# Optimization experiments

Hardware: AMD Instinct MI355X
Metric: run time of the kernel (lower is better)

The kernel has to match this reference:

```python
import jax, jax.numpy as jnp
import numpy as np

N_NODES = 100000
N_EDGES = 1000000
C_IN = 64
C_OUT = 64


def setup_inputs() -> dict:
    key = jax.random.key(0)
    k1, k2, k3 = jax.random.split(key, 3)
    x = jax.random.normal(k1, (N_NODES, C_IN), dtype=jnp.float32)
    edge_index = jax.random.randint(k2, (2, N_EDGES), 0, N_NODES, dtype=jnp.int64)
    # glorot-scaled weight, zero bias (as in GCNConv defaults)
    scale = jnp.sqrt(2.0 / (C_IN + C_OUT)).astype(jnp.float32)
    W = jax.random.normal(k3, (C_IN, C_OUT), dtype=jnp.float32) * scale
    b = jnp.zeros((C_OUT,), dtype=jnp.float32)
    return {"x": x, "edge_index": edge_index, "W": W, "b": b}


def reference(x, edge_index, W, b):
    # GCNConv: out = D^{-1/2} (A + I) D^{-1/2} (x W) + b
    n = x.shape[0]
    # add self loops
    loop = jnp.arange(n, dtype=edge_index.dtype)
    src = jnp.concatenate([edge_index[0], loop])  # [E+N]
    dst = jnp.concatenate([edge_index[1], loop])  # [E+N]
    # degree of A_hat computed over destination (col) nodes, edge_weight = 1
    ones = jnp.ones(src.shape[0], dtype=x.dtype)
    deg = jax.ops.segment_sum(ones, dst, num_segments=n)  # [N]
    deg_inv_sqrt = jnp.where(deg > 0, jax.lax.rsqrt(deg), 0.0)
    norm = deg_inv_sqrt[src] * deg_inv_sqrt[dst]  # [E+N]
    # linear transform, then gather-scale-scatter aggregation
    h = x @ W  # [N, C_OUT]
    msg = norm[:, None] * h[src]  # [E+N, C_OUT]
    out = jax.ops.segment_sum(msg, dst, num_segments=n)  # [N, C_OUT]
    return out + b
```

## Files before the change

kernel.cpp:

```cpp
#include <hip/hip_runtime.h>
#include <hip/hip_bf16.h>

#define C 64

__device__ __forceinline__ float bflo(unsigned u) { return __uint_as_float(u << 16); }
__device__ __forceinline__ float bfhi(unsigned u) { return __uint_as_float(u & 0xffff0000u); }
__device__ __forceinline__ unsigned bfrne(float f) {
    unsigned u = __float_as_uint(f);
    return (u + 0x7fffu + ((u >> 16) & 1u)) >> 16;
}

__device__ __forceinline__ unsigned xcc_id() {
    return __builtin_amdgcn_s_getreg(6164) & 7u;
}

__global__ void zero_kernel(uint4* __restrict__ p, int n4) {
    int i = blockIdx.x * blockDim.x + threadIdx.x;
    if (i < n4) p[i] = make_uint4(0u, 0u, 0u, 0u);
}

__global__ void count_part_kernel(const int* __restrict__ dst, unsigned* __restrict__ part,
                                  int S, unsigned* __restrict__ rank, int E) {
    int e = blockIdx.x * blockDim.x + threadIdx.x;
    if (e < E) {
        unsigned x = xcc_id();
        unsigned d = (unsigned)dst[e];
        unsigned r = __hip_atomic_fetch_add(&part[x * (unsigned)S + d], 1u,
                                            __ATOMIC_RELAXED, __HIP_MEMORY_SCOPE_WORKGROUP);
        rank[e] = (x << 27) | r;
    }
}

__global__ void scan1_kernel(unsigned* __restrict__ part, int S,
                             unsigned* __restrict__ deg, unsigned* __restrict__ offs,
                             unsigned* __restrict__ bsum, float* __restrict__ dis, int n) {
    __shared__ unsigned s[256];
    int t = threadIdx.x;
    int base = blockIdx.x * 1024 + t * 4;
    unsigned v0 = 0, v1 = 0, v2 = 0, v3 = 0;
    if (base + 4 <= n) {
        uint4 run = make_uint4(0u, 0u, 0u, 0u);
        #pragma unroll
        for (int x = 0; x < 8; ++x) {
            uint4* p = (uint4*)&part[(size_t)x * S + base];
            uint4 v = *p;
            *p = run;
            run.x += v.x; run.y += v.y; run.z += v.z; run.w += v.w;
        }
        v0 = run.x; v1 = run.y; v2 = run.z; v3 = run.w;
        *(uint4*)&deg[base] = run;
        dis[base + 0] = rsqrtf((float)(v0 + 1u));
        dis[base + 1] = rsqrtf((float)(v1 + 1u));
        dis[base + 2] = rsqrtf((float)(v2 + 1u));
        dis[base + 3] = rsqrtf((float)(v3 + 1u));
    } else if (base < n) {
        for (int j = 0; j < 4; ++j) {
            int i = base + j;
            if (i >= n) break;
            unsigned run = 0;
            #pragma unroll
            for (int x = 0; x < 8; ++x) {
                unsigned* p = &part[(size_t)x * S + i];
                unsigned v = *p;
                *p = run;
                run += v;
            }
            deg[i] = run;
            dis[i] = rsqrtf((float)(run + 1u));
            if (j == 0) v0 = run; else if (j == 1) v1 = run;
            else if (j == 2) v2 = run; else v3 = run;
        }
    }
    s[t] = v0 + v1 + v2 + v3;
    __syncthreads();
    for (int d = 1; d < 256; d <<= 1) {
        unsigned val = (t >= d) ? s[t - d] : 0u;
        __syncthreads();
        s[t] += val;
        __syncthreads();
    }
    unsigned excl = (t == 0) ? 0u : s[t - 1];
    if (t == 255) bsum[blockIdx.x] = s[255];
    if (base + 0 < n) offs[base + 0] = excl;
    if (base + 1 < n) offs[base + 1] = excl + v0;
    if (base + 2 < n) offs[base + 2] = excl + v0 + v1;
    if (base + 3 < n) offs[base + 3] = excl + v0 + v1 + v2;
}

__global__ void scan2_kernel(unsigned* __restrict__ bsum, int nb) {
    __shared__ unsigned s[256];
    int t = threadIdx.x;
    s[t] = (t < nb) ? bsum[t] : 0u;
    __syncthreads();
    for (int d = 1; d < 256; d <<= 1) {
        unsigned val = (t >= d) ? s[t - d] : 0u;
        __syncthreads();
        s[t] += val;
        __syncthreads();
    }
    if (t < nb) bsum[t] = (t == 0) ? 0u : s[t - 1];
}

__global__ void bucket_kernel(const int* __restrict__ src, const int* __restrict__ dst,
                              const unsigned* __restrict__ offs, const unsigned* __restrict__ bsum,
                              const unsigned* __restrict__ part, int S,
                              const unsigned* __restrict__ rank, unsigned* __restrict__ ssrc, int E) {
    int e = blockIdx.x * blockDim.x + threadIdx.x;
    if (e < E) {
        unsigned d = (unsigned)dst[e];
        unsigned u = rank[e];
        unsigned x = u >> 27;
        unsigned pos = offs[d] + bsum[d >> 10] + part[(size_t)x * S + d] + (u & 0x07FFFFFFu);
        ssrc[pos] = (unsigned)src[e];
    }
}

__global__ void __launch_bounds__(256, 4)
gemm64_kernel(const float* __restrict__ x, const float* __restrict__ W,
              const float* __restrict__ dis, unsigned short* __restrict__ hsb, int n) {
    __shared__ float Xl[64][68];
    __shared__ float Wl[64][64];
    int tid = threadIdx.x;
    int rbase = blockIdx.x * 64;
    for (int i = tid; i < 1024; i += 256) {
        ((float4*)Wl)[i] = ((const float4*)W)[i];
    }
    for (int i = tid; i < 1024; i += 256) {
        int r = i >> 4, kq = i & 15;
        float4 v;
        if (rbase + r < n) v = ((const float4*)(x + (size_t)(rbase + r) * C))[kq];
        else               v = make_float4(0.f, 0.f, 0.f, 0.f);
        *(float4*)&Xl[r][kq * 4] = v;
    }
    __syncthreads();

    int tx = tid & 15;
    int ty = tid >> 4;
    float4 acc[4];
    #pragma unroll
    for (int j = 0; j < 4; ++j) acc[j] = make_float4(0.f, 0.f, 0.f, 0.f);

    #pragma unroll 2
    for (int kb = 0; kb < 16; ++kb) {
        float4 wv0 = *(const float4*)&Wl[kb * 4 + 0][tx * 4];
        float4 wv1 = *(const float4*)&Wl[kb * 4 + 1][tx * 4];
        float4 wv2 = *(const float4*)&Wl[kb * 4 + 2][tx * 4];
        float4 wv3 = *(const float4*)&Wl[kb * 4 + 3][tx * 4];
        #pragma unroll
        for (int j = 0; j < 4; ++j) {
            float4 xv = *(const float4*)&Xl[ty * 4 + j][kb * 4];
            acc[j].x = fmaf(xv.x, wv0.x, acc[j].x);
            acc[j].y = fmaf(xv.x, wv0.y, acc[j].y);
            acc[j].z = fmaf(xv.x, wv0.z, acc[j].z);
            acc[j].w = fmaf(xv.x, wv0.w, acc[j].w);
            acc[j].x = fmaf(xv.y, wv1.x, acc[j].x);
            acc[j].y = fmaf(xv.y, wv1.y, acc[j].y);
            acc[j].z = fmaf(xv.y, wv1.z, acc[j].z);
            acc[j].w = fmaf(xv.y, wv1.w, acc[j].w);
            acc[j].x = fmaf(xv.z, wv2.x, acc[j].x);
            acc[j].y = fmaf(xv.z, wv2.y, acc[j].y);
            acc[j].z = fmaf(xv.z, wv2.z, acc[j].z);
            acc[j].w = fmaf(xv.z, wv2.w, acc[j].w);
            acc[j].x = fmaf(xv.w, wv3.x, acc[j].x);
            acc[j].y = fmaf(xv.w, wv3.y, acc[j].y);
            acc[j].z = fmaf(xv.w, wv3.z, acc[j].z);
            acc[j].w = fmaf(xv.w, wv3.w, acc[j].w);
        }
    }
    #pragma unroll
    for (int j = 0; j < 4; ++j) {
        int row = rbase + ty * 4 + j;
        if (row < n) {
            float d = dis[row];
            unsigned p0 = bfrne(acc[j].x * d) | (bfrne(acc[j].y * d) << 16);
            unsigned p1 = bfrne(acc[j].z * d) | (bfrne(acc[j].w * d) << 16);
            ((uint2*)(hsb + (size_t)row * C))[tx] = make_uint2(p0, p1);
        }
    }
}

__global__ void gather_kernel(const unsigned* __restrict__ offs, const unsigned* __restrict__ bsum,
                              const unsigned* __restrict__ deg, const unsigned* __restrict__ ssrc,
                              const float* __restrict__ dis, const unsigned short* __restrict__ hsb,
                              const float* __restrict__ b, float* __restrict__ out, int n) {
    int node = blockIdx.x * 4 + (threadIdx.x >> 6);
    if (node >= n) return;
    int lane = threadIdx.x & 63;
    int g = lane >> 3;
    int l = lane & 7;
    unsigned off = offs[node] + bsum[node >> 10];
    unsigned dg  = deg[node];
    float a0 = 0.f, a1 = 0.f, a2 = 0.f, a3 = 0.f, a4 = 0.f, a5 = 0.f, a6 = 0.f, a7 = 0.f;
    unsigned k = 0;
    for (; k + 16 <= dg; k += 16) {
        unsigned s0 = ssrc[off + k + g];
        unsigned s1 = ssrc[off + k + 8 + g];
        uint4 v0 = ((const uint4*)(hsb + (size_t)s0 * C))[l];
        uint4 v1 = ((const uint4*)(hsb + (size_t)s1 * C))[l];
        a0 += bflo(v0.x) + bflo(v1.x); a1 += bfhi(v0.x) + bfhi(v1.x);
        a2 += bflo(v0.y) + bflo(v1.y); a3 += bfhi(v0.y) + bfhi(v1.y);
        a4 += bflo(v0.z) + bflo(v1.z); a5 += bfhi(v0.z) + bfhi(v1.z);
        a6 += bflo(v0.w) + bflo(v1.w); a7 += bfhi(v0.w) + bfhi(v1.w);
    }
    if (k + 8 <= dg) {
        unsigned s0 = ssrc[off + k + g];
        uint4 v0 = ((const uint4*)(hsb + (size_t)s0 * C))[l];
        a0 += bflo(v0.x); a1 += bfhi(v0.x);
        a2 += bflo(v0.y); a3 += bfhi(v0.y);
        a4 += bflo(v0.z); a5 += bfhi(v0.z);
        a6 += bflo(v0.w); a7 += bfhi(v0.w);
        k += 8;
    }
    if (k + g < dg) {
        unsigned s0 = ssrc[off + k + g];
        uint4 v0 = ((const uint4*)(hsb + (size_t)s0 * C))[l];
        a0 += bflo(v0.x); a1 += bfhi(v0.x);
        a2 += bflo(v0.y); a3 += bfhi(v0.y);
        a4 += bflo(v0.z); a5 += bfhi(v0.z);
        a6 += bflo(v0.w); a7 += bfhi(v0.w);
    }
    #pragma unroll
    for (int m = 8; m <= 32; m <<= 1) {
        a0 += __shfl_xor(a0, m); a1 += __shfl_xor(a1, m);
        a2 += __shfl_xor(a2, m); a3 += __shfl_xor(a3, m);
        a4 += __shfl_xor(a4, m); a5 += __shfl_xor(a5, m);
        a6 += __shfl_xor(a6, m); a7 += __shfl_xor(a7, m);
    }
    if (g < 2) {
        float di = dis[node];
        uint4 u = ((const uint4*)(hsb + (size_t)node * C))[l];
        unsigned w0 = (g == 0) ? u.x : u.z;
        unsigned w1 = (g == 0) ? u.y : u.w;
        float s0 = bflo(w0), s1 = bfhi(w0), s2 = bflo(w1), s3 = bfhi(w1);
        float e0 = (g == 0) ? a0 : a4;
        float e1 = (g == 0) ? a1 : a5;
        float e2 = (g == 0) ? a2 : a6;
        float e3 = (g == 0) ? a3 : a7;
        float4 bv = ((const float4*)b)[l * 2 + g];
        float4 o;
        o.x = di * (s0 + e0) + bv.x;
        o.y = di * (s1 + e1) + bv.y;
        o.z = di * (s2 + e2) + bv.z;
        o.w = di * (s3 + e3) + bv.w;
        ((float4*)(out + (size_t)node * C))[l * 2 + g] = o;
    }
}

extern "C" void kernel_launch(void* const* d_in, const int* in_sizes, int n_in,
                              void* d_out, int out_size, void* d_ws, size_t ws_size,
                              hipStream_t stream) {
    const float* x   = (const float*)d_in[0];
    const int*   ei  = (const int*)d_in[1];
    const float* W   = (const float*)d_in[2];
    const float* b   = (const float*)d_in[3];
    float*       out = (float*)d_out;

    const int N = in_sizes[0] / C;
    const int E = in_sizes[1] / 2;
    const int* src = ei;
    const int* dst = ei + E;

    const int S = (N + 63) & ~63;

    char* ws = (char*)d_ws;
    size_t o = 0;
    auto carve = [&](size_t bytes) { char* p = ws + o; o = (o + bytes + 255) & ~(size_t)255; return p; };
    unsigned* part      = (unsigned*)carve((size_t)8 * S * 4);
    unsigned* deg       = (unsigned*)carve((size_t)N * 4);
    unsigned* offs      = (unsigned*)carve((size_t)N * 4);
    unsigned* bsum      = (unsigned*)carve(1024 * 4);
    float*    dis       = (float*)carve((size_t)N * 4);
    unsigned* rank      = (unsigned*)carve((size_t)E * 4);
    unsigned* ssrc      = (unsigned*)carve((size_t)E * 4);
    unsigned short* hsb = (unsigned short*)carve((size_t)N * C * 2);

    int n4 = 2 * S;
    zero_kernel<<<(n4 + 255) / 256, 256, 0, stream>>>((uint4*)part, n4);

    count_part_kernel<<<(E + 255) / 256, 256, 0, stream>>>(dst, part, S, rank, E);

    int nb = (N + 1023) / 1024;
    scan1_kernel<<<nb, 256, 0, stream>>>(part, S, deg, offs, bsum, dis, N);
    scan2_kernel<<<1, 256, 0, stream>>>(bsum, nb);

    bucket_kernel<<<(E + 255) / 256, 256, 0, stream>>>(src, dst, offs, bsum, part, S, rank, ssrc, E);

    gemm64_kernel<<<(N + 63) / 64, 256, 0, stream>>>(x, W, dis, hsb, N);

    gather_kernel<<<(N + 3) / 4, 256, 0, stream>>>(offs, bsum, deg, ssrc, dis, hsb, b, out, N);
}
```

Before: 131.2 us.

## Fuse CSR build kernels into one cooperative kernel with grid syncs

Merges the zero, count, two scan and bucket kernels into a single cooperative kernel launched with 1024 blocks, using grid.sync between phases instead of separate launches. This is meant to remove four kernel launch gaps and their tail effects. In exchange it adds grid-wide barrier costs and grid-stride loops over fewer threads, and it relies on all 1024 blocks being co-resident.

```diff
diff --git a/kernel.cpp b/kernel.cpp
--- a/kernel.cpp
+++ b/kernel.cpp
@@ -1,7 +1,11 @@
 #include <hip/hip_runtime.h>
 #include <hip/hip_bf16.h>
+#include <hip/hip_cooperative_groups.h>
+
+namespace cg = cooperative_groups;
 
 #define C 64
+#define COOP_BLOCKS 1024
 
 __device__ __forceinline__ float bflo(unsigned u) { return __uint_as_float(u << 16); }
 __device__ __forceinline__ float bfhi(unsigned u) { return __uint_as_float(u & 0xffff0000u); }
@@ -14,99 +18,105 @@
     return __builtin_amdgcn_s_getreg(6164) & 7u;
 }
 
-__global__ void zero_kernel(uint4* __restrict__ p, int n4) {
-    int i = blockIdx.x * blockDim.x + threadIdx.x;
-    if (i < n4) p[i] = make_uint4(0u, 0u, 0u, 0u);
-}
-
-__global__ void count_part_kernel(const int* __restrict__ dst, unsigned* __restrict__ part,
-                                  int S, unsigned* __restrict__ rank, int E) {
-    int e = blockIdx.x * blockDim.x + threadIdx.x;
-    if (e < E) {
+__global__ void __launch_bounds__(256, 8)
+build_kernel(const int* __restrict__ dst, const int* __restrict__ src,
+             unsigned* __restrict__ part, int S,
+             unsigned* __restrict__ rank,
+             unsigned* __restrict__ deg, unsigned* __restrict__ offs,
+             unsigned* __restrict__ bsum, float* __restrict__ dis,
+             unsigned* __restrict__ ssrc, int N, int E) {
+    cg::grid_group grid = cg::this_grid();
+    __shared__ unsigned s[256];
+    int t    = threadIdx.x;
+    int gtid = blockIdx.x * 256 + t;
+    int gsz  = gridDim.x * 256;
+
+    int n4 = 2 * S;
+    for (int i = gtid; i < n4; i += gsz) {
+        ((uint4*)part)[i] = make_uint4(0u, 0u, 0u, 0u);
+    }
+    grid.sync();
+
+    {
         unsigned x = xcc_id();
-        unsigned d = (unsigned)dst[e];
-        unsigned r = __hip_atomic_fetch_add(&part[x * (unsigned)S + d], 1u,
-                                            __ATOMIC_RELAXED, __HIP_MEMORY_SCOPE_WORKGROUP);
-        rank[e] = (x << 27) | r;
-    }
-}
-
-__global__ void scan1_kernel(unsigned* __restrict__ part, int S,
-                             unsigned* __restrict__ deg, unsigned* __restrict__ offs,
-                             unsigned* __restrict__ bsum, float* __restrict__ dis, int n) {
-    __shared__ unsigned s[256];
-    int t = threadIdx.x;
-    int base = blockIdx.x * 1024 + t * 4;
-    unsigned v0 = 0, v1 = 0, v2 = 0, v3 = 0;
-    if (base + 4 <= n) {
-        uint4 run = make_uint4(0u, 0u, 0u, 0u);
-        #pragma unroll
-        for (int x = 0; x < 8; ++x) {
-            uint4* p = (uint4*)&part[(size_t)x * S + base];
-            uint4 v = *p;
-            *p = run;
-            run.x += v.x; run.y += v.y; run.z += v.z; run.w += v.w;
-        }
-        v0 = run.x; v1 = run.y; v2 = run.z; v3 = run.w;
-        *(uint4*)&deg[base] = run;
-        dis[base + 0] = rsqrtf((float)(v0 + 1u));
-        dis[base + 1] = rsqrtf((float)(v1 + 1u));
-        dis[base + 2] = rsqrtf((float)(v2 + 1u));
-        dis[base + 3] = rsqrtf((float)(v3 + 1u));
-    } else if (base < n) {
-        for (int j = 0; j < 4; ++j) {
-            int i = base + j;
-            if (i >= n) break;
-            unsigned run = 0;
+        for (int e = gtid; e < E; e += gsz) {
+            unsigned d = (unsigned)dst[e];
+            unsigned r = __hip_atomic_fetch_add(&part[x * (unsigned)S + d], 1u,
+                                                __ATOMIC_RELAXED, __HIP_MEMORY_SCOPE_WORKGROUP);
+            rank[e] = (x << 27) | r;
+        }
+    }
+    grid.sync();
+
+    int nchunks = (N + 1023) >> 10;
+    for (int c = blockIdx.x; c < nchunks; c += gridDim.x) {
+        int base = c * 1024 + t * 4;
+        unsigned v0 = 0, v1 = 0, v2 = 0, v3 = 0;
+        if (base + 4 <= N) {
+            uint4 run = make_uint4(0u, 0u, 0u, 0u);
             #pragma unroll
             for (int x = 0; x < 8; ++x) {
-                unsigned* p = &part[(size_t)x * S + i];
-                unsigned v = *p;
+                uint4* p = (uint4*)&part[(size_t)x * S + base];
+                uint4 v = *p;
                 *p = run;
-                run += v;
+                run.x += v.x; run.y += v.y; run.z += v.z; run.w += v.w;
             }
-            deg[i] = run;
-            dis[i] = rsqrtf((float)(run + 1u));
-            if (j == 0) v0 = run; else if (j == 1) v1 = run;
-            else if (j == 2) v2 = run; else v3 = run;
-        }
-    }
-    s[t] = v0 + v1 + v2 + v3;
-    __syncthreads();
-    for (int d = 1; d < 256; d <<= 1) {
-        unsigned val = (t >= d) ? s[t - d] : 0u;
+            v0 = run.x; v1 = run.y; v2 = run.z; v3 = run.w;
+            *(uint4*)&deg[base] = run;
+            dis[base + 0] = rsqrtf((float)(v0 + 1u));
+            dis[base + 1] = rsqrtf((float)(v1 + 1u));
+            dis[base + 2] = rsqrtf((float)(v2 + 1u));
+            dis[base + 3] = rsqrtf((float)(v3 + 1u));
+        } else if (base < N) {
+            for (int j = 0; j < 4; ++j) {
+                int i = base + j;
+                if (i >= N) break;
+                unsigned run = 0;
+                #pragma unroll
+                for (int x = 0; x < 8; ++x) {
+                    unsigned* p = &part[(size_t)x * S + i];
+                    unsigned v = *p;
+                    *p = run;
+                    run += v;
+                }
+                deg[i] = run;
+                dis[i] = rsqrtf((float)(run + 1u));
+                if (j == 0) v0 = run; else if (j == 1) v1 = run;
+                else if (j == 2) v2 = run; else v3 = run;
+            }
+        }
+        s[t] = v0 + v1 + v2 + v3;
         __syncthreads();
-        s[t] += val;
+        for (int d = 1; d < 256; d <<= 1) {
+            unsigned val = (t >= d) ? s[t - d] : 0u;
+            __syncthreads();
+            s[t] += val;
+            __syncthreads();
+        }
+        unsigned excl = (t == 0) ? 0u : s[t - 1];
+        if (t == 255) bsum[c] = s[255];
+        if (base + 0 < N) offs[base + 0] = excl;
+        if (base + 1 < N) offs[base + 1] = excl + v0;
+        if (base + 2 < N) offs[base + 2] = excl + v0 + v1;
+        if (base + 3 < N) offs[base + 3] = excl + v0 + v1 + v2;
         __syncthreads();
     }
-    unsigned excl = (t == 0) ? 0u : s[t - 1];
-    if (t == 255) bsum[blockIdx.x] = s[255];
-    if (base + 0 < n) offs[base + 0] = excl;
-    if (base + 1 < n) offs[base + 1] = excl + v0;
-    if (base + 2 < n) offs[base + 2] = excl + v0 + v1;
-    if (base + 3 < n) offs[base + 3] = excl + v0 + v1 + v2;
-}
-
-__global__ void scan2_kernel(unsigned* __restrict__ bsum, int nb) {
-    __shared__ unsigned s[256];
-    int t = threadIdx.x;
-    s[t] = (t < nb) ? bsum[t] : 0u;
-    __syncthreads();
-    for (int d = 1; d < 256; d <<= 1) {
-        unsigned val = (t >= d) ? s[t - d] : 0u;
+    grid.sync();
+
+    if (blockIdx.x == 0) {
+        s[t] = (t < nchunks) ? bsum[t] : 0u;
         __syncthreads();
-        s[t] += val;
-        __syncthreads();
-    }
-    if (t < nb) bsum[t] = (t == 0) ? 0u : s[t - 1];
-}
-
-__global__ void bucket_kernel(const int* __restrict__ src, const int* __restrict__ dst,
-                              const unsigned* __restrict__ offs, const unsigned* __restrict__ bsum,
-                              const unsigned* __restrict__ part, int S,
-                              const unsigned* __restrict__ rank, unsigned* __restrict__ ssrc, int E) {
-    int e = blockIdx.x * blockDim.x + threadIdx.x;
-    if (e < E) {
+        for (int d = 1; d < 256; d <<= 1) {
+            unsigned val = (t >= d) ? s[t - d] : 0u;
+            __syncthreads();
+            s[t] += val;
+            __syncthreads();
+        }
+        if (t < nchunks) bsum[t] = (t == 0) ? 0u : s[t - 1];
+    }
+    grid.sync();
+
+    for (int e = gtid; e < E; e += gsz) {
         unsigned d = (unsigned)dst[e];
         unsigned u = rank[e];
         unsigned x = u >> 27;
@@ -274,16 +284,24 @@
     unsigned* ssrc      = (unsigned*)carve((size_t)E * 4);
     unsigned short* hsb = (unsigned short*)carve((size_t)N * C * 2);
 
-    int n4 = 2 * S;
-    zero_kernel<<<(n4 + 255) / 256, 256, 0, stream>>>((uint4*)part, n4);
-
-    count_part_kernel<<<(E + 255) / 256, 256, 0, stream>>>(dst, part, S, rank, E);
-
-    int nb = (N + 1023) / 1024;
-    scan1_kernel<<<nb, 256, 0, stream>>>(part, S, deg, offs, bsum, dis, N);
-    scan2_kernel<<<1, 256, 0, stream>>>(bsum, nb);
-
-    bucket_kernel<<<(E + 255) / 256, 256, 0, stream>>>(src, dst, offs, bsum, part, S, rank, ssrc, E);
+    {
+        const int*  dst_a  = dst;
+        const int*  src_a  = src;
+        unsigned*   part_a = part;
+        int         S_a    = S;
+        unsigned*   rank_a = rank;
+        unsigned*   deg_a  = deg;
+        unsigned*   offs_a = offs;
+        unsigned*   bsum_a = bsum;
+        float*      dis_a  = dis;
+        unsigned*   ssrc_a = ssrc;
+        int         N_a    = N;
+        int         E_a    = E;
+        void* args[] = { &dst_a, &src_a, &part_a, &S_a, &rank_a, &deg_a,
+                         &offs_a, &bsum_a, &dis_a, &ssrc_a, &N_a, &E_a };
+        hipLaunchCooperativeKernel((const void*)build_kernel,
+                                   dim3(COOP_BLOCKS), dim3(256), args, 0, stream);
+    }
 
     gemm64_kernel<<<(N + 63) / 64, 256, 0, stream>>>(x, W, dis, hsb, N);
 
```

Result: slower. 507.3 us (+286.8%).

## Fuse degree scan with GEMM, drop second scan kernel, vectorize edge kernels

Applied to the files above, without the earlier changes.

Merges the per-chunk degree scan and the dense x@W GEMM into one kernel that handles 256 nodes per block, so the separate scan2 and gemm launches go away. Each consumer now rebuilds the chunk prefix itself: bucket_kernel scans all 391 chunk sums in shared memory per block, and gather_kernel reduces bsum up to its chunk per block. The count and bucket kernels process four edges per thread using uint4 loads. The cost is redundant prefix work in every block of bucket and gather, plus fewer, heavier GEMM blocks.

```diff
diff --git a/kernel.cpp b/kernel.cpp
--- a/kernel.cpp
+++ b/kernel.cpp
@@ -21,160 +21,179 @@
 
 __global__ void count_part_kernel(const int* __restrict__ dst, unsigned* __restrict__ part,
                                   int S, unsigned* __restrict__ rank, int E) {
-    int e = blockIdx.x * blockDim.x + threadIdx.x;
-    if (e < E) {
-        unsigned x = xcc_id();
-        unsigned d = (unsigned)dst[e];
-        unsigned r = __hip_atomic_fetch_add(&part[x * (unsigned)S + d], 1u,
-                                            __ATOMIC_RELAXED, __HIP_MEMORY_SCOPE_WORKGROUP);
-        rank[e] = (x << 27) | r;
-    }
-}
-
-__global__ void scan1_kernel(unsigned* __restrict__ part, int S,
-                             unsigned* __restrict__ deg, unsigned* __restrict__ offs,
-                             unsigned* __restrict__ bsum, float* __restrict__ dis, int n) {
+    int g = blockIdx.x * blockDim.x + threadIdx.x;
+    int e0 = g * 4;
+    if (e0 >= E) return;
+    unsigned x = xcc_id();
+    unsigned xbase = x * (unsigned)S;
+    if (e0 + 4 <= E) {
+        uint4 d4 = ((const uint4*)dst)[g];
+        uint4 r4;
+        r4.x = (x << 27) | __hip_atomic_fetch_add(&part[xbase + d4.x], 1u, __ATOMIC_RELAXED, __HIP_MEMORY_SCOPE_WORKGROUP);
+        r4.y = (x << 27) | __hip_atomic_fetch_add(&part[xbase + d4.y], 1u, __ATOMIC_RELAXED, __HIP_MEMORY_SCOPE_WORKGROUP);
+        r4.z = (x << 27) | __hip_atomic_fetch_add(&part[xbase + d4.z], 1u, __ATOMIC_RELAXED, __HIP_MEMORY_SCOPE_WORKGROUP);
+        r4.w = (x << 27) | __hip_atomic_fetch_add(&part[xbase + d4.w], 1u, __ATOMIC_RELAXED, __HIP_MEMORY_SCOPE_WORKGROUP);
+        ((uint4*)rank)[g] = r4;
+    } else {
+        for (int e = e0; e < E; ++e) {
+            unsigned d = (unsigned)dst[e];
+            unsigned r = __hip_atomic_fetch_add(&part[xbase + d], 1u, __ATOMIC_RELAXED, __HIP_MEMORY_SCOPE_WORKGROUP);
+            rank[e] = (x << 27) | r;
+        }
+    }
+}
+
+__global__ void __launch_bounds__(256, 4)
+scan_gemm_kernel(unsigned* __restrict__ part, int S,
+                 const float* __restrict__ x, const float* __restrict__ W,
+                 unsigned* __restrict__ deg, unsigned* __restrict__ offs,
+                 unsigned* __restrict__ bsum, float* __restrict__ dis,
+                 unsigned short* __restrict__ hsb, int N) {
+    __shared__ float Wl[64][64];
+    __shared__ float Xl[64][68];
     __shared__ unsigned s[256];
+    __shared__ float sdis[256];
     int t = threadIdx.x;
-    int base = blockIdx.x * 1024 + t * 4;
-    unsigned v0 = 0, v1 = 0, v2 = 0, v3 = 0;
-    if (base + 4 <= n) {
-        uint4 run = make_uint4(0u, 0u, 0u, 0u);
+    int nbase = blockIdx.x * 256;
+
+    for (int i = t; i < 1024; i += 256) {
+        ((float4*)Wl)[i] = ((const float4*)W)[i];
+    }
+
+    int i = nbase + t;
+    unsigned degv = 0;
+    if (i < N) {
+        unsigned run = 0;
         #pragma unroll
-        for (int x = 0; x < 8; ++x) {
-            uint4* p = (uint4*)&part[(size_t)x * S + base];
-            uint4 v = *p;
+        for (int xx = 0; xx < 8; ++xx) {
+            unsigned* p = &part[(size_t)xx * S + i];
+            unsigned v = *p;
             *p = run;
-            run.x += v.x; run.y += v.y; run.z += v.z; run.w += v.w;
-        }
-        v0 = run.x; v1 = run.y; v2 = run.z; v3 = run.w;
-        *(uint4*)&deg[base] = run;
-        dis[base + 0] = rsqrtf((float)(v0 + 1u));
-        dis[base + 1] = rsqrtf((float)(v1 + 1u));
-        dis[base + 2] = rsqrtf((float)(v2 + 1u));
-        dis[base + 3] = rsqrtf((float)(v3 + 1u));
-    } else if (base < n) {
-        for (int j = 0; j < 4; ++j) {
-            int i = base + j;
-            if (i >= n) break;
-            unsigned run = 0;
-            #pragma unroll
-            for (int x = 0; x < 8; ++x) {
-                unsigned* p = &part[(size_t)x * S + i];
-                unsigned v = *p;
-                *p = run;
-                run += v;
-            }
-            deg[i] = run;
-            dis[i] = rsqrtf((float)(run + 1u));
-            if (j == 0) v0 = run; else if (j == 1) v1 = run;
-            else if (j == 2) v2 = run; else v3 = run;
-        }
-    }
-    s[t] = v0 + v1 + v2 + v3;
+            run += v;
+        }
+        degv = run;
+        deg[i] = run;
+        float dv = rsqrtf((float)(run + 1u));
+        dis[i] = dv;
+        sdis[t] = dv;
+    } else {
+        sdis[t] = 0.f;
+    }
+    s[t] = degv;
     __syncthreads();
     for (int d = 1; d < 256; d <<= 1) {
-        unsigned val = (t >= d) ? s[t - d] : 0u;
-        __syncthreads();
-        s[t] += val;
-        __syncthreads();
-    }
-    unsigned excl = (t == 0) ? 0u : s[t - 1];
+        unsigned v = (t >= d) ? s[t - d] : 0u;
+        __syncthreads();
+        s[t] += v;
+        __syncthreads();
+    }
+    if (i < N) offs[i] = s[t] - degv;
     if (t == 255) bsum[blockIdx.x] = s[255];
-    if (base + 0 < n) offs[base + 0] = excl;
-    if (base + 1 < n) offs[base + 1] = excl + v0;
-    if (base + 2 < n) offs[base + 2] = excl + v0 + v1;
-    if (base + 3 < n) offs[base + 3] = excl + v0 + v1 + v2;
-}
-
-__global__ void scan2_kernel(unsigned* __restrict__ bsum, int nb) {
-    __shared__ unsigned s[256];
-    int t = threadIdx.x;
-    s[t] = (t < nb) ? bsum[t] : 0u;
     __syncthreads();
-    for (int d = 1; d < 256; d <<= 1) {
-        unsigned val = (t >= d) ? s[t - d] : 0u;
-        __syncthreads();
-        s[t] += val;
-        __syncthreads();
-    }
-    if (t < nb) bsum[t] = (t == 0) ? 0u : s[t - 1];
-}
-
-__global__ void bucket_kernel(const int* __restrict__ src, const int* __restrict__ dst,
-                              const unsigned* __restrict__ offs, const unsigned* __restrict__ bsum,
-                              const unsigned* __restrict__ part, int S,
-                              const unsigned* __restrict__ rank, unsigned* __restrict__ ssrc, int E) {
-    int e = blockIdx.x * blockDim.x + threadIdx.x;
-    if (e < E) {
-        unsigned d = (unsigned)dst[e];
-        unsigned u = rank[e];
-        unsigned x = u >> 27;
-        unsigned pos = offs[d] + bsum[d >> 10] + part[(size_t)x * S + d] + (u & 0x07FFFFFFu);
-        ssrc[pos] = (unsigned)src[e];
-    }
-}
-
-__global__ void __launch_bounds__(256, 4)
-gemm64_kernel(const float* __restrict__ x, const float* __restrict__ W,
-              const float* __restrict__ dis, unsigned short* __restrict__ hsb, int n) {
-    __shared__ float Xl[64][68];
-    __shared__ float Wl[64][64];
-    int tid = threadIdx.x;
-    int rbase = blockIdx.x * 64;
-    for (int i = tid; i < 1024; i += 256) {
-        ((float4*)Wl)[i] = ((const float4*)W)[i];
-    }
-    for (int i = tid; i < 1024; i += 256) {
-        int r = i >> 4, kq = i & 15;
-        float4 v;
-        if (rbase + r < n) v = ((const float4*)(x + (size_t)(rbase + r) * C))[kq];
-        else               v = make_float4(0.f, 0.f, 0.f, 0.f);
-        *(float4*)&Xl[r][kq * 4] = v;
-    }
-    __syncthreads();
-
-    int tx = tid & 15;
-    int ty = tid >> 4;
-    float4 acc[4];
-    #pragma unroll
-    for (int j = 0; j < 4; ++j) acc[j] = make_float4(0.f, 0.f, 0.f, 0.f);
-
-    #pragma unroll 2
-    for (int kb = 0; kb < 16; ++kb) {
-        float4 wv0 = *(const float4*)&Wl[kb * 4 + 0][tx * 4];
-        float4 wv1 = *(const float4*)&Wl[kb * 4 + 1][tx * 4];
-        float4 wv2 = *(const float4*)&Wl[kb * 4 + 2][tx * 4];
-        float4 wv3 = *(const float4*)&Wl[kb * 4 + 3][tx * 4];
+
+    int tx = t & 15;
+    int ty = t >> 4;
+    for (int tile = 0; tile < 4; ++tile) {
+        int rbase = nbase + tile * 64;
+        if (rbase >= N) break;
+        for (int ii = t; ii < 1024; ii += 256) {
+            int r = ii >> 4, kq = ii & 15;
+            float4 v;
+            if (rbase + r < N) v = ((const float4*)(x + (size_t)(rbase + r) * C))[kq];
+            else               v = make_float4(0.f, 0.f, 0.f, 0.f);
+            *(float4*)&Xl[r][kq * 4] = v;
+        }
+        __syncthreads();
+        float4 acc[4];
+        #pragma unroll
+        for (int j = 0; j < 4; ++j) acc[j] = make_float4(0.f, 0.f, 0.f, 0.f);
+        #pragma unroll 2
+        for (int kb = 0; kb < 16; ++kb) {
+            float4 wv0 = *(const float4*)&Wl[kb * 4 + 0][tx * 4];
+            float4 wv1 = *(const float4*)&Wl[kb * 4 + 1][tx * 4];
+            float4 wv2 = *(const float4*)&Wl[kb * 4 + 2][tx * 4];
+            float4 wv3 = *(const float4*)&Wl[kb * 4 + 3][tx * 4];
+            #pragma unroll
+            for (int j = 0; j < 4; ++j) {
+                float4 xv = *(const float4*)&Xl[ty * 4 + j][kb * 4];
+                acc[j].x = fmaf(xv.x, wv0.x, acc[j].x);
+                acc[j].y = fmaf(xv.x, wv0.y, acc[j].y);
+                acc[j].z = fmaf(xv.x, wv0.z, acc[j].z);
+                acc[j].w = fmaf(xv.x, wv0.w, acc[j].w);
+                acc[j].x = fmaf(xv.y, wv1.x, acc[j].x);
+                acc[j].y = fmaf(xv.y, wv1.y, acc[j].y);
+                acc[j].z = fmaf(xv.y, wv1.z, acc[j].z);
+                acc[j].w = fmaf(xv.y, wv1.w, acc[j].w);
+                acc[j].x = fmaf(xv.z, wv2.x, acc[j].x);
+                acc[j].y = fmaf(xv.z, wv2.y, acc[j].y);
+                acc[j].z = fmaf(xv.z, wv2.z, acc[j].z);
+                acc[j].w = fmaf(xv.z, wv2.w, acc[j].w);
+                acc[j].x = fmaf(xv.w, wv3.x, acc[j].x);
+                acc[j].y = fmaf(xv.w, wv3.y, acc[j].y);
+                acc[j].z = fmaf(xv.w, wv3.z, acc[j].z);
+                acc[j].w = fmaf(xv.w, wv3.w, acc[j].w);
+            }
+        }
         #pragma unroll
         for (int j = 0; j < 4; ++j) {
-            float4 xv = *(const float4*)&Xl[ty * 4 + j][kb * 4];
-            acc[j].x = fmaf(xv.x, wv0.x, acc[j].x);
-            acc[j].y = fmaf(xv.x, wv0.y, acc[j].y);
-            acc[j].z = fmaf(xv.x, wv0.z, acc[j].z);
-            acc[j].w = fmaf(xv.x, wv0.w, acc[j].w);
-            acc[j].x = fmaf(xv.y, wv1.x, acc[j].x);
-            acc[j].y = fmaf(xv.y, wv1.y, acc[j].y);
-            acc[j].z = fmaf(xv.y, wv1.z, acc[j].z);
-            acc[j].w = fmaf(xv.y, wv1.w, acc[j].w);
-            acc[j].x = fmaf(xv.z, wv2.x, acc[j].x);
-            acc[j].y = fmaf(xv.z, wv2.y, acc[j].y);
-            acc[j].z = fmaf(xv.z, wv2.z, acc[j].z);
-            acc[j].w = fmaf(xv.z, wv2.w, acc[j].w);
-            acc[j].x = fmaf(xv.w, wv3.x, acc[j].x);
-            acc[j].y = fmaf(xv.w, wv3.y, acc[j].y);
-            acc[j].z = fmaf(xv.w, wv3.z, acc[j].z);
-            acc[j].w = fmaf(xv.w, wv3.w, acc[j].w);
-        }
-    }
-    #pragma unroll
-    for (int j = 0; j < 4; ++j) {
-        int row = rbase + ty * 4 + j;
-        if (row < n) {
-            float d = dis[row];
-            unsigned p0 = bfrne(acc[j].x * d) | (bfrne(acc[j].y * d) << 16);
-            unsigned p1 = bfrne(acc[j].z * d) | (bfrne(acc[j].w * d) << 16);
-            ((uint2*)(hsb + (size_t)row * C))[tx] = make_uint2(p0, p1);
+            int row = rbase + ty * 4 + j;
+            if (row < N) {
+                float d = sdis[tile * 64 + ty * 4 + j];
+                unsigned p0 = bfrne(acc[j].x * d) | (bfrne(acc[j].y * d) << 16);
+                unsigned p1 = bfrne(acc[j].z * d) | (bfrne(acc[j].w * d) << 16);
+                ((uint2*)(hsb + (size_t)row * C))[tx] = make_uint2(p0, p1);
+            }
+        }
+        __syncthreads();
+    }
+}
+
+__global__ void __launch_bounds__(256)
+bucket_kernel(const int* __restrict__ src, const int* __restrict__ dst,
+              const unsigned* __restrict__ offs, const unsigned* __restrict__ bsum,
+              const unsigned* __restrict__ part, int S,
+              const unsigned* __restrict__ rank, unsigned* __restrict__ ssrc,
+              int E, int nch) {
+    __shared__ unsigned sb[512];
+    int t = threadIdx.x;
+    sb[t]       = (t < nch)       ? bsum[t]       : 0u;
+    sb[t + 256] = (t + 256 < nch) ? bsum[t + 256] : 0u;
+    __syncthreads();
+    for (int d = 1; d < 512; d <<= 1) {
+        unsigned v0 = (t >= d) ? sb[t - d] : 0u;
+        unsigned v1 = sb[t + 256 - d];
+        __syncthreads();
+        sb[t] += v0;
+        sb[t + 256] += v1;
+        __syncthreads();
+    }
+    int g = blockIdx.x * 256 + t;
+    int e0 = g * 4;
+    if (e0 >= E) return;
+    if (e0 + 4 <= E) {
+        uint4 d4 = ((const uint4*)dst)[g];
+        uint4 s4 = ((const uint4*)src)[g];
+        uint4 r4 = ((const uint4*)rank)[g];
+        #define PLACE(dd, ss, uu) { \
+            unsigned ch = (dd) >> 8; \
+            unsigned pre = ch ? sb[ch - 1] : 0u; \
+            unsigned xx = (uu) >> 27; \
+            unsigned pos = offs[dd] + pre + part[(size_t)xx * S + (dd)] + ((uu) & 0x07FFFFFFu); \
+            ssrc[pos] = (ss); }
+        PLACE(d4.x, s4.x, r4.x);
+        PLACE(d4.y, s4.y, r4.y);
+        PLACE(d4.z, s4.z, r4.z);
+        PLACE(d4.w, s4.w, r4.w);
+        #undef PLACE
+    } else {
+        for (int e = e0; e < E; ++e) {
+            unsigned dd = (unsigned)dst[e];
+            unsigned uu = rank[e];
+            unsigned ch = dd >> 8;
+            unsigned pre = ch ? sb[ch - 1] : 0u;
+            unsigned xx = uu >> 27;
+            unsigned pos = offs[dd] + pre + part[(size_t)xx * S + dd] + (uu & 0x07FFFFFFu);
+            ssrc[pos] = (unsigned)src[e];
         }
     }
 }
@@ -183,12 +202,27 @@
                               const unsigned* __restrict__ deg, const unsigned* __restrict__ ssrc,
                               const float* __restrict__ dis, const unsigned short* __restrict__ hsb,
                               const float* __restrict__ b, float* __restrict__ out, int n) {
-    int node = blockIdx.x * 4 + (threadIdx.x >> 6);
+    __shared__ unsigned sred[256];
+    int t = threadIdx.x;
+    int node0 = blockIdx.x * 4;
+    int c0 = node0 >> 8;
+    unsigned partial = 0;
+    for (int i = t; i < c0; i += 256) partial += bsum[i];
+    sred[t] = partial;
+    __syncthreads();
+    #pragma unroll
+    for (int d = 128; d > 0; d >>= 1) {
+        if (t < d) sred[t] += sred[t + d];
+        __syncthreads();
+    }
+    unsigned pref = sred[0];
+
+    int node = node0 + (t >> 6);
     if (node >= n) return;
-    int lane = threadIdx.x & 63;
+    int lane = t & 63;
     int g = lane >> 3;
     int l = lane & 7;
-    unsigned off = offs[node] + bsum[node >> 10];
+    unsigned off = offs[node] + pref;
     unsigned dg  = deg[node];
     float a0 = 0.f, a1 = 0.f, a2 = 0.f, a3 = 0.f, a4 = 0.f, a5 = 0.f, a6 = 0.f, a7 = 0.f;
     unsigned k = 0;
@@ -261,6 +295,7 @@
     const int* dst = ei + E;
 
     const int S = (N + 63) & ~63;
+    const int nch = (N + 255) >> 8;
 
     char* ws = (char*)d_ws;
     size_t o = 0;
@@ -277,15 +312,12 @@
     int n4 = 2 * S;
     zero_kernel<<<(n4 + 255) / 256, 256, 0, stream>>>((uint4*)part, n4);
 
-    count_part_kernel<<<(E + 255) / 256, 256, 0, stream>>>(dst, part, S, rank, E);
-
-    int nb = (N + 1023) / 1024;
-    scan1_kernel<<<nb, 256, 0, stream>>>(part, S, deg, offs, bsum, dis, N);
-    scan2_kernel<<<1, 256, 0, stream>>>(bsum, nb);
-
-    bucket_kernel<<<(E + 255) / 256, 256, 0, stream>>>(src, dst, offs, bsum, part, S, rank, ssrc, E);
-
-    gemm64_kernel<<<(N + 63) / 64, 256, 0, stream>>>(x, W, dis, hsb, N);
+    int ng = (E + 3) / 4;
+    count_part_kernel<<<(ng + 255) / 256, 256, 0, stream>>>(dst, part, S, rank, E);
+
+    scan_gemm_kernel<<<nch, 256, 0, stream>>>(part, S, x, W, deg, offs, bsum, dis, hsb, N);
+
+    bucket_kernel<<<(ng + 255) / 256, 256, 0, stream>>>(src, dst, offs, bsum, part, S, rank, ssrc, E, nch);
 
     gather_kernel<<<(N + 3) / 4, 256, 0, stream>>>(offs, bsum, deg, ssrc, dis, hsb, b, out, N);
 }
```

New measurement: 148.1 us. +12.9%, slower.
